# Kernel optimization log

Hardware: AMD Instinct MI355X
Metric: run time of the kernel (lower is better)

Reference implementation:

```python
import jax, jax.numpy as jnp
import numpy as np

T, B, D, H = 512, 128, 512, 512

def setup_inputs() -> dict:
    key = jax.random.key(0)
    k1, k2, k3, k4 = jax.random.split(key, 4)
    s_in = 1.0 / np.sqrt(D)
    s_h = 1.0 / np.sqrt(H)
    return {
        "x": jax.random.normal(k1, (T, B, D), dtype=jnp.float32),
        "resets": jax.random.randint(k2, (T, B), 0, 2) > 0,
        "h0": jnp.zeros((B, H), dtype=jnp.float32),  # GRUCell.initialize_carry -> zeros
        "Wi": jax.random.normal(k3, (D, 3 * H), dtype=jnp.float32) * s_in,  # [ir|iz|in]
        "bi": jnp.zeros((3 * H,), dtype=jnp.float32),
        "Wh": jax.random.normal(k4, (H, 3 * H), dtype=jnp.float32) * s_h,  # [hr|hz|hn]
        "bhn": jnp.zeros((H,), dtype=jnp.float32),
    }

def reference(x, resets, h0, Wi, bi, Wh, bhn):
    # Precompute all input-side gate projections in one big GEMM: [T,B,3H]
    xg = jnp.einsum('tbd,dk->tbk', x, Wi) + bi

    def step(h, inp):
        xg_t, reset_t = inp
        # reset masking: replace carry with fresh zero carry where episode resets
        h = jnp.where(reset_t[:, None], jnp.zeros_like(h), h)
        hg = h @ Wh  # [B,3H]
        xr, xz, xn = jnp.split(xg_t, 3, axis=-1)
        hr, hz, hn = jnp.split(hg, 3, axis=-1)
        r = jax.nn.sigmoid(xr + hr)
        z = jax.nn.sigmoid(xz + hz)
        n = jnp.tanh(xn + r * (hn + bhn))
        h_new = (1.0 - z) * n + z * h
        return h_new, h_new

    h_final, ys = jax.lax.scan(step, h0, (xg, resets))
    return h_final, ys
```

## Files before the change

kernel.cpp:

```cpp
#include <hip/hip_runtime.h>

typedef __attribute__((ext_vector_type(4))) float f32x4;
typedef __attribute__((ext_vector_type(8))) _Float16 f16x8;
typedef __attribute__((ext_vector_type(4))) _Float16 f16x4;
typedef unsigned short u16;
typedef unsigned int u32;
typedef unsigned long long u64;

#define XGCAP 34304
#define NXG 4096

__device__ __forceinline__ float sigm(float v){ return 1.0f / (1.0f + __expf(-v)); }
__device__ __forceinline__ float tanh_fast(float v){
  v = fminf(15.0f, fmaxf(-15.0f, v));
  float e = __expf(2.0f * v);
  return (e - 1.0f) / (e + 1.0f);
}
__device__ __forceinline__ void gload16(const void* g, void* l){
  __builtin_amdgcn_global_load_lds((const __attribute__((address_space(1))) void*)g,
                                   (__attribute__((address_space(3))) void*)l, 16, 0, 0);
}
__device__ __forceinline__ double aload(const double* p){
  return __hip_atomic_load(p, __ATOMIC_RELAXED, __HIP_MEMORY_SCOPE_AGENT);
}
__device__ __forceinline__ void astore(float* p, float v){
  __hip_atomic_store(p, v, __ATOMIC_RELAXED, __HIP_MEMORY_SCOPE_AGENT);
}
__device__ __forceinline__ u32 apoll(const u32* p){
  return __hip_atomic_load(p, __ATOMIC_RELAXED, __HIP_MEMORY_SCOPE_AGENT);
}
__device__ __forceinline__ void abump(u32* p, u32 v){
  __hip_atomic_fetch_add(p, v, __ATOMIC_RELAXED, __HIP_MEMORY_SCOPE_AGENT);
}
__device__ __forceinline__ float2 d2f2(double d){ union{double d; float2 f;} u; u.d = d; return u.f; }

__global__ __launch_bounds__(512) void prep_lists(
    const void* __restrict__ resets_raw, const float* __restrict__ h0,
    u32* __restrict__ rows, u32* __restrict__ off, int* __restrict__ nlists)
{
  __shared__ u64 cb[128][8];
  __shared__ u32 cnt8[8][512];
  __shared__ u32 cnt[520];
  __shared__ u32 offs[521];
  __shared__ u32 cur[520];
  __shared__ int is_bytes, h0nz, maxli;
  const int tid = threadIdx.x;
  const int b = tid & 127, tc = tid >> 7;
  for (int i = tid; i < 520; i += 512){ cnt[i] = 0; cur[i] = 0; }
  if (tid == 0){ is_bytes = 0; h0nz = 0; maxli = 0; }
  for (int i = tid; i < 64; i += 512) rows[65536 + i] = (2u << 16);
  __syncthreads();
  {
    const u32* w = (const u32*)resets_raw;
    int bad = 0;
    for (int i = tid; i < 4096; i += 512) bad |= (w[i] > 1u);
    if (bad) atomicOr(&is_bytes, 1);
  }
  {
    const u32* hw = (const u32*)h0;
    u32 o = 0;
    for (int i = tid; i < 65536; i += 512) o |= hw[i];
    if (o) atomicOr(&h0nz, 1);
  }
  __syncthreads();
  const bool h0zero = (h0nz == 0);
  u64 bits0 = 0, bits1 = 0;
  if (is_bytes){
    const unsigned char* ru8 = (const unsigned char*)resets_raw;
    for (int i = 0; i < 128; ++i){
      int t = tc*128 + i;
      if (ru8[t*128 + b]){
        if (i < 64) bits0 |= 1ull << i; else bits1 |= 1ull << (i - 64);
      }
    }
  } else {
    const u32* ri32 = (const u32*)resets_raw;
    for (int i = 0; i < 128; ++i){
      int t = tc*128 + i;
      if (ri32[t*128 + b]){
        if (i < 64) bits0 |= 1ull << i; else bits1 |= 1ull << (i - 64);
      }
    }
  }
  cb[b][tc*2]     = bits0;
  cb[b][tc*2 + 1] = bits1;
  __syncthreads();

#define CELL_LI() \
    u64 myw = (i < 64) ? bits0 : bits1; \
    int rs = (int)((myw >> (i & 63)) & 1ull); \
    int k = t >> 6; \
    u64 m = cb[b][k] | (k == 0 ? 1ull : 0ull); \
    int r6 = t & 63; \
    m &= (r6 == 63) ? ~0ull : ((1ull << (r6 + 1)) - 1ull); \
    while (m == 0ull){ --k; m = cb[b][k] | (k == 0 ? 1ull : 0ull); } \
    int lastE = (k << 6) + 63 - (int)__builtin_clzll(m); \
    int depth = t - lastE; \
    int li = (depth == 0) ? ((rs || h0zero) ? 0 : 1) : (depth + 1);

  {
    u64 cpack = 0;
    int lmax = 0;
    for (int i = 0; i < 128; ++i){
      const int t = tc*128 + i;
      CELL_LI();
      if (li > lmax) lmax = li;
      if (li < 8) cpack += 1ull << (li * 8);
      else atomicAdd(&cnt[li], 1u);
    }
    atomicMax(&maxli, lmax);
    #pragma unroll
    for (int l = 0; l < 8; ++l) cnt8[l][tid] = (u32)((cpack >> (l * 8)) & 0xFFull);
  }
  __syncthreads();
  if (tid < 8){
    u32 s = 0;
    for (int i = 0; i < 512; ++i){ u32 v = cnt8[tid][i]; cnt8[tid][i] = s; s += v; }
    cnt[tid] = s;
  }
  __syncthreads();
  if (tid == 0){
    u32 s = 0;
    for (int i = 0; i < 520; ++i){ offs[i] = s; s += cnt[i]; }
    offs[520] = s;
    *nlists = maxli + 1;
  }
  __syncthreads();
  for (int i = tid; i < 521; i += 512) off[i] = offs[i];
  __syncthreads();
  {
    u64 lcpack = 0;
    for (int i = 0; i < 128; ++i){
      const int t = tc*128 + i;
      CELL_LI();
      u32 p;
      if (li < 8){
        u32 loc = (u32)((lcpack >> (li * 8)) & 0xFFull);
        lcpack += 1ull << (li * 8);
        p = offs[li] + cnt8[li][tid] + loc;
      } else {
        p = offs[li] + atomicAdd(&cur[li], 1u);
      }
      u32 fl = rs ? 1u : ((t == 0) ? (h0zero ? 1u : 2u) : 0u);
      rows[p] = (u32)t | ((u32)b << 9) | (fl << 16);
    }
  }
#undef CELL_LI
}

__global__ void prep_w(const float* __restrict__ Wi, const float* __restrict__ Wh,
                       char* __restrict__ wimg, u32* __restrict__ zflags)
{
  if (blockIdx.x < 128){
    #pragma unroll
    for (int i = 0; i < 4; ++i)
      zflags[blockIdx.x * 1024 + (int)threadIdx.x + i * 256] = 0;
  }
  __shared__ float tile[64][65];
  const int bc = blockIdx.x % 24;
  const int bk = blockIdx.x / 24;
  const int scol0 = (bc % 3) * 512 + (bc / 3) * 64;
  const int k0 = bk * 64;
  #pragma unroll
  for (int i = 0; i < 4; ++i){
    int idx = (int)threadIdx.x + i*256;
    int kk = idx >> 4, c4 = idx & 15;
    int k = k0 + kk;
    const float* src = (k < 512) ? (Wi + (size_t)k*1536 + scol0 + c4*4)
                                 : (Wh + (size_t)(k-512)*1536 + scol0 + c4*4);
    float4 v = *(const float4*)src;
    tile[kk][c4*4+0] = v.x; tile[kk][c4*4+1] = v.y;
    tile[kk][c4*4+2] = v.z; tile[kk][c4*4+3] = v.w;
  }
  __syncthreads();
  const int jb = bc / 3;
  #pragma unroll
  for (int i = 0; i < 4; ++i){
    int idx = (int)threadIdx.x + i*256;
    int cc = idx >> 4, k4 = idx & 15;
    int cimg = (bc % 3)*64 + cc;
    f16x4 c;
    c[0] = (_Float16)tile[k4*4+0][cc]; c[1] = (_Float16)tile[k4*4+1][cc];
    c[2] = (_Float16)tile[k4*4+2][cc]; c[3] = (_Float16)tile[k4*4+3][cc];
    int bby = k4*8;
    int sb = (bby & 8) | ((bby & 0x70) ^ ((cimg & 7) << 4));
    *(f16x4*)(wimg + ((size_t)(jb*16 + bk))*24576 + cimg*128 + sb) = c;
  }
}

__global__ __launch_bounds__(256) void prep_x(
    const float* __restrict__ x, const u32* __restrict__ rows,
    char* __restrict__ xq)
{
  const int tid = threadIdx.x;
  const u32 lpos = blockIdx.x * 16 + (tid >> 4);
  const u32 e = rows[lpos];
  const float* src = x + ((size_t)((e & 511u)*128u + ((e >> 9) & 127u)))*512;
  const int lane16 = tid & 15;
  char* dst = xq + (size_t)lpos * 1024;
  const int swzr = ((int)lpos & 7) << 4;
  #pragma unroll
  for (int it = 0; it < 8; ++it){
    float4 v = *(const float4*)(src + it*64 + lane16*4);
    f16x4 c; c[0]=(_Float16)v.x; c[1]=(_Float16)v.y;
             c[2]=(_Float16)v.z; c[3]=(_Float16)v.w;
    int bby = lane16 * 8;
    int sb = (bby & 8) | ((bby & 0x70) ^ swzr);
    *(f16x4*)(dst + it*128 + sb) = c;
  }
}

__global__ __launch_bounds__(256, 2) void gru_fused(
    const char* __restrict__ xq, const float* __restrict__ bi,
    const float* __restrict__ bhn, const char* __restrict__ wimg,
    const float* __restrict__ h0, _Float16* __restrict__ xg,
    const u32* __restrict__ rows, const u32* __restrict__ off,
    const int* __restrict__ nlists, u32* __restrict__ hflags,
    u32* __restrict__ xflags, float* __restrict__ out)
{
  __shared__ __align__(16) char smem[81920];
  float* ys = out + 65536;
  const u32 n0 = off[1];
  const int tid = threadIdx.x;
  const int lane = tid & 63, wave = tid >> 6;
  const int nblk = (int)gridDim.x;

  int g = (int)blockIdx.x;
  while (g < NXG){
    const int tm = g >> 3, jb = g & 7;
    g += nblk;
    const char* asrc = xq + (size_t)tm * 131072;
    const char* wsrc = wimg + ((size_t)jb * 16) * 24576;

    f32x4 acc[3][8];
    #pragma unroll
    for (int c = 0; c < 3; ++c)
      #pragma unroll
      for (int m = 0; m < 8; ++m) acc[c][m] = (f32x4){0.f,0.f,0.f,0.f};

#define DMA_A(KC, BUF) do{ \
    char* l_ = smem + (BUF)*16384 + wave*4096; \
    const char* g_ = asrc + (size_t)(wave*32 + (lane>>3))*1024 + (KC)*128 + (lane&7)*16; \
    _Pragma("unroll") for (int i_ = 0; i_ < 4; ++i_) \
      gload16(g_ + i_*8192, l_ + i_*1024); }while(0)
#define DMA_W(KC, BUF) do{ \
    char* l_ = smem + 32768 + (BUF)*24576 + wave*6144; \
    const char* g_ = wsrc + (size_t)(KC)*24576 + wave*6144 + lane*16; \
    _Pragma("unroll") for (int i_ = 0; i_ < 6; ++i_) \
      gload16(g_ + i_*1024, l_ + i_*1024); }while(0)

    DMA_A(0, 0); DMA_W(0, 0);
    __syncthreads();
    for (int kc = 0; kc < 8; ++kc){
      const int cur = kc & 1;
      if (kc < 7){ DMA_A(kc+1, cur^1); DMA_W(kc+1, cur^1); }
      const char* Ab = smem + cur*16384;
      const char* Wb = smem + 32768 + cur*24576;
      #pragma unroll
      for (int kk = 0; kk < 2; ++kk){
        const int bby = kk*64 + (lane>>4)*16;
        f16x8 af[8];
        #pragma unroll
        for (int mi = 0; mi < 8; ++mi){
          int rr = mi*16 + (lane & 15);
          af[mi] = *(const f16x8*)(Ab + rr*128 + (bby ^ ((rr & 7) << 4)));
        }
        #pragma unroll
        for (int cls = 0; cls < 3; ++cls){
          int cc = cls*64 + wave*16 + (lane & 15);
          f16x8 wf = *(const f16x8*)(Wb + cc*128 + (bby ^ ((cc & 7) << 4)));
          #pragma unroll
          for (int mi = 0; mi < 8; ++mi)
            acc[cls][mi] = __builtin_amdgcn_mfma_f32_16x16x32_f16(af[mi], wf, acc[cls][mi], 0, 0, 0);
        }
      }
      __syncthreads();
    }
#undef DMA_A
#undef DMA_W

    const int jloc = wave*16 + (lane & 15);
    const int j = jb*64 + jloc;
    const float bir = bi[j], biz = bi[512 + j], bin = bi[1024 + j], bh = bhn[j];
    #pragma unroll
    for (int mi = 0; mi < 8; ++mi){
      #pragma unroll
      for (int rg = 0; rg < 4; ++rg){
        int r = mi*16 + (lane >> 4)*4 + rg;
        u32 e = rows[tm*128 + r];
        int tt = (int)(e & 511u), bb = (int)((e >> 9) & 127u);
        float xr = acc[0][mi][rg] + bir;
        float xz = acc[1][mi][rg] + biz;
        float xn = acc[2][mi][rg] + bin;
        if ((e >> 16) == 1u){
          float rr = sigm(xr), zz = sigm(xz);
          float nn = tanh_fast(xn + rr*bh);
          float hv = (1.f - zz)*nn;
          ys[((size_t)(tt*128 + bb))*512 + j] = hv;
          if (tt == 511) out[(size_t)bb*512 + j] = hv;
        } else {
          u32 xi = (u32)(tm*128 + r) - n0;
          if (xi >= XGCAP) xi = 0;
          _Float16* p = xg + (size_t)xi*1536 + jb*192 + jloc;
          p[0]   = (_Float16)xr;
          p[64]  = (_Float16)xz;
          p[128] = (_Float16)xn;
        }
      }
    }
    __syncthreads();
    if (tid < 128){
      u32 e = rows[tm*128 + tid];
      if ((e >> 16) == 1u) abump(&hflags[(e & 511u)*128u + ((e >> 9) & 127u)], 1u);
      else                 abump(&xflags[tm*128 + tid], 1u);
    }
    __syncthreads();
  }

  const int L = *nlists;
  int myNext = g - NXG;
  int gt = 0;
  for (int li = 1; li < L; ++li){
    const u32 offA = off[li];
    const int nA = (int)(off[li+1] - offA);
    const int tA = (nA + 63) >> 6;
    const int nt = tA * 8;
    while (myNext < gt + nt){
      const int tile = myNext - gt;
      myNext += nblk;
      const int tm = tile >> 3, jb = tile & 7;
      const u32 rowbase = offA + (u32)tm*64u;
      const u32 xibase = rowbase - n0;
      const int mcount = min(64, nA - tm*64);
      const char* wp = wimg + ((size_t)jb*16 + 8)*24576;
      const int jloc = wave*16 + (lane & 15);

      if (wave == 0 && lane < mcount){
        u32 e = rows[rowbase + lane];
        const bool needH = ((e >> 16) == 0u);
        u32 hidx = ((e & 511u) - 1u)*128u + ((e >> 9) & 127u);
        int guard = 0;
        for (;;){
          bool ok = apoll(&xflags[rowbase + lane]) >= 8u;
          if (ok && needH) ok = apoll(&hflags[hidx]) >= 8u;
          if (ok) break;
          __builtin_amdgcn_s_sleep(1);
          if (++guard > (1 << 20)) break;
        }
      }
      __syncthreads();

      const float* rp[4];
      #pragma unroll
      for (int i = 0; i < 4; ++i){
        u32 e = rows[rowbase + (tid>>4) + i*16];
        int tt = (int)(e & 511u), bb = (int)((e >> 9) & 127u);
        const float* base = ((e >> 16) == 0u) ? (ys + ((size_t)((tt-1)*128 + bb))*512)
                                              : (h0 + (size_t)bb*512);
        rp[i] = base + (tid & 15)*4;
      }

      _Float16 xgp[3][4][4];
      #pragma unroll
      for (int mi = 0; mi < 4; ++mi){
        #pragma unroll
        for (int rg = 0; rg < 4; ++rg){
          u32 xi = xibase + (u32)(mi*16 + (lane >> 4)*4 + rg);
          if (xi >= XGCAP) xi = 0;
          const _Float16* p = xg + (size_t)xi*1536 + jb*192 + jloc;
          xgp[0][mi][rg] = p[0];
          xgp[1][mi][rg] = p[64];
          xgp[2][mi][rg] = p[128];
        }
      }

      f32x4 acc[3][4];
      #pragma unroll
      for (int c = 0; c < 3; ++c)
        #pragma unroll
        for (int m = 0; m < 4; ++m) acc[c][m] = (f32x4){0.f,0.f,0.f,0.f};
      float hp[4][4];
      double s0[4][2], s1[4][2], s2[4][2];

#define ALOAD(S, CK) do{ \
    _Pragma("unroll") for (int i_ = 0; i_ < 4; ++i_){ \
      const double* p_ = (const double*)(rp[i_] + (CK)*64); \
      S[i_][0] = aload(p_); S[i_][1] = aload(p_ + 1); } }while(0)

#define AWRITE(S, CK) do{ \
    char* An_ = smem + ((CK) & 3)*8192; \
    _Pragma("unroll") for (int i_ = 0; i_ < 4; ++i_){ \
      float2 u0_ = d2f2(S[i_][0]), u1_ = d2f2(S[i_][1]); \
      int r_ = (tid>>4) + i_*16, bby_ = (tid & 15)*8; \
      int sb_ = (bby_ & 8) | ((bby_ & 0x70) ^ ((r_ & 7) << 4)); \
      f16x4 c_; c_[0]=(_Float16)u0_.x; c_[1]=(_Float16)u0_.y; \
                c_[2]=(_Float16)u1_.x; c_[3]=(_Float16)u1_.y; \
      *(f16x4*)(An_ + r_*128 + sb_) = c_; } }while(0)

#define COMPUTE(KC) do{ \
    const char* Ab_ = smem + ((KC) & 3)*8192; \
    _Pragma("unroll") for (int kk_ = 0; kk_ < 2; ++kk_){ \
      const int bby_ = kk_*64 + (lane>>4)*16; \
      f16x8 af_[4]; \
      _Pragma("unroll") for (int mi_ = 0; mi_ < 4; ++mi_){ \
        int rr_ = mi_*16 + (lane & 15); \
        af_[mi_] = *(const f16x8*)(Ab_ + rr_*128 + (bby_ ^ ((rr_ & 7) << 4))); } \
      _Pragma("unroll") for (int cl_ = 0; cl_ < 3; ++cl_){ \
        int cc_ = cl_*64 + wave*16 + (lane & 15); \
        f16x8 wf_ = *(const f16x8*)(wp + (size_t)(KC)*24576 + cc_*128 + (bby_ ^ ((cc_ & 7) << 4))); \
        _Pragma("unroll") for (int mi_ = 0; mi_ < 4; ++mi_) \
          acc[cl_][mi_] = __builtin_amdgcn_mfma_f32_16x16x32_f16(af_[mi_], wf_, acc[cl_][mi_], 0, 0, 0); } } \
    if ((KC) == jb){ \
      const int bb2_ = jloc*2; \
      _Pragma("unroll") for (int mi_ = 0; mi_ < 4; ++mi_) \
        _Pragma("unroll") for (int rg_ = 0; rg_ < 4; ++rg_){ \
          int r2_ = mi_*16 + (lane >> 4)*4 + rg_; \
          int sb2_ = (bb2_ & 0x0F) | ((bb2_ & 0x70) ^ ((r2_ & 7) << 4)); \
          hp[mi_][rg_] = (float)(*(const _Float16*)(Ab_ + r2_*128 + sb2_)); } } }while(0)

      ALOAD(s0, 0); ALOAD(s1, 1); ALOAD(s2, 2);
      AWRITE(s0, 0);
      __syncthreads();
      ALOAD(s0, 3); COMPUTE(0); AWRITE(s1, 1); __syncthreads();
      ALOAD(s1, 4); COMPUTE(1); AWRITE(s2, 2); __syncthreads();
      ALOAD(s2, 5); COMPUTE(2); AWRITE(s0, 3); __syncthreads();
      ALOAD(s0, 6); COMPUTE(3); AWRITE(s1, 4); __syncthreads();
      ALOAD(s1, 7); COMPUTE(4); AWRITE(s2, 5); __syncthreads();
                    COMPUTE(5); AWRITE(s0, 6); __syncthreads();
                    COMPUTE(6); AWRITE(s1, 7); __syncthreads();
                    COMPUTE(7);
#undef ALOAD
#undef AWRITE
#undef COMPUTE

      const int j = jb*64 + jloc;
      const float bh = bhn[j];
      #pragma unroll
      for (int mi = 0; mi < 4; ++mi){
        #pragma unroll
        for (int rg = 0; rg < 4; ++rg){
          int r = mi*16 + (lane >> 4)*4 + rg;
          if (r < mcount){
            u32 e = rows[rowbase + r];
            int tt = (int)(e & 511u), bb = (int)((e >> 9) & 127u);
            float rr = sigm((float)xgp[0][mi][rg] + acc[0][mi][rg]);
            float zz = sigm((float)xgp[1][mi][rg] + acc[1][mi][rg]);
            float nn = tanh_fast((float)xgp[2][mi][rg] + rr*(acc[2][mi][rg] + bh));
            float hv = (1.f - zz)*nn + zz*hp[mi][rg];
            astore(&ys[((size_t)(tt*128 + bb))*512 + j], hv);
            if (tt == 511) out[(size_t)bb*512 + j] = hv;
          }
        }
      }
      __syncthreads();
      if (tid < mcount){
        u32 e = rows[rowbase + tid];
        abump(&hflags[(e & 511u)*128u + ((e >> 9) & 127u)], 1u);
      }
    }
    gt += nt;
  }
}

extern "C" void kernel_launch(void* const* d_in, const int* in_sizes, int n_in,
                              void* d_out, int out_size, void* d_ws, size_t ws_size,
                              hipStream_t stream)
{
  const float* x  = (const float*)d_in[0];
  const void*  resets = d_in[1];
  const float* h0 = (const float*)d_in[2];
  const float* Wi = (const float*)d_in[3];
  const float* bi = (const float*)d_in[4];
  const float* Wh = (const float*)d_in[5];
  const float* bhn= (const float*)d_in[6];
  float* out = (float*)d_out;

  char* ws = (char*)d_ws;
  u32* off    = (u32*)ws;
  int* nlists = (int*)(ws + 4096);
  u32* rows   = (u32*)(ws + 8192);
  u32* hflags = (u32*)(ws + 294912);
  u32* xflags = (u32*)(ws + 557056);
  char* wimg  = ws + 819200;
  char* xq    = ws + 4194304;
  _Float16* xg = (_Float16*)(ws + 71303168);

  prep_lists<<<dim3(1), dim3(512), 0, stream>>>(resets, h0, rows, off, nlists);
  prep_w<<<dim3(384), dim3(256), 0, stream>>>(Wi, Wh, wimg, hflags);
  prep_x<<<dim3(4096), dim3(256), 0, stream>>>(x, rows, xq);

  int perCU = 0;
  (void)hipOccupancyMaxActiveBlocksPerMultiprocessor(&perCU, gru_fused, 256, 0);
  if (perCU < 1) perCU = 1;
  int grid = perCU * 256;
  if (grid > 1024) grid = 1024;

  void* args[] = {(void*)&xq, (void*)&bi, (void*)&bhn, (void*)&wimg,
                  (void*)&h0, (void*)&xg, (void*)&rows, (void*)&off,
                  (void*)&nlists, (void*)&hflags, (void*)&xflags, (void*)&out};
  hipLaunchCooperativeKernel(gru_fused, dim3(grid), dim3(256), args, 0, stream);

  (void)in_sizes; (void)n_in; (void)out_size; (void)ws_size;
}
```

Baseline: 931.2 us.

## Merge weight and input prep kernels; read GEMM weights directly from global

```diff
diff --git a/kernel.cpp b/kernel.cpp
--- a/kernel.cpp
+++ b/kernel.cpp
@@ -148,13 +148,35 @@
 #undef CELL_LI
 }
 
-__global__ void prep_w(const float* __restrict__ Wi, const float* __restrict__ Wh,
-                       char* __restrict__ wimg, u32* __restrict__ zflags)
+__global__ __launch_bounds__(256) void prep_wx(
+    const float* __restrict__ Wi, const float* __restrict__ Wh,
+    char* __restrict__ wimg, u32* __restrict__ zflags,
+    const float* __restrict__ x, const u32* __restrict__ rows,
+    char* __restrict__ xq)
 {
+  const int tid = threadIdx.x;
+  if (blockIdx.x >= 384){
+    const u32 lpos = (blockIdx.x - 384) * 16 + (tid >> 4);
+    const u32 e = rows[lpos];
+    const float* src = x + ((size_t)((e & 511u)*128u + ((e >> 9) & 127u)))*512;
+    const int lane16 = tid & 15;
+    char* dst = xq + (size_t)lpos * 1024;
+    const int swzr = ((int)lpos & 7) << 4;
+    #pragma unroll
+    for (int it = 0; it < 8; ++it){
+      float4 v = *(const float4*)(src + it*64 + lane16*4);
+      f16x4 c; c[0]=(_Float16)v.x; c[1]=(_Float16)v.y;
+               c[2]=(_Float16)v.z; c[3]=(_Float16)v.w;
+      int bby = lane16 * 8;
+      int sb = (bby & 8) | ((bby & 0x70) ^ swzr);
+      *(f16x4*)(dst + it*128 + sb) = c;
+    }
+    return;
+  }
   if (blockIdx.x < 128){
     #pragma unroll
     for (int i = 0; i < 4; ++i)
-      zflags[blockIdx.x * 1024 + (int)threadIdx.x + i * 256] = 0;
+      zflags[blockIdx.x * 1024 + tid + i * 256] = 0;
   }
   __shared__ float tile[64][65];
   const int bc = blockIdx.x % 24;
@@ -163,7 +185,7 @@
   const int k0 = bk * 64;
   #pragma unroll
   for (int i = 0; i < 4; ++i){
-    int idx = (int)threadIdx.x + i*256;
+    int idx = tid + i*256;
     int kk = idx >> 4, c4 = idx & 15;
     int k = k0 + kk;
     const float* src = (k < 512) ? (Wi + (size_t)k*1536 + scol0 + c4*4)
@@ -176,7 +198,7 @@
   const int jb = bc / 3;
   #pragma unroll
   for (int i = 0; i < 4; ++i){
-    int idx = (int)threadIdx.x + i*256;
+    int idx = tid + i*256;
     int cc = idx >> 4, k4 = idx & 15;
     int cimg = (bc % 3)*64 + cc;
     f16x4 c;
@@ -188,28 +210,6 @@
   }
 }
 
-__global__ __launch_bounds__(256) void prep_x(
-    const float* __restrict__ x, const u32* __restrict__ rows,
-    char* __restrict__ xq)
-{
-  const int tid = threadIdx.x;
-  const u32 lpos = blockIdx.x * 16 + (tid >> 4);
-  const u32 e = rows[lpos];
-  const float* src = x + ((size_t)((e & 511u)*128u + ((e >> 9) & 127u)))*512;
-  const int lane16 = tid & 15;
-  char* dst = xq + (size_t)lpos * 1024;
-  const int swzr = ((int)lpos & 7) << 4;
-  #pragma unroll
-  for (int it = 0; it < 8; ++it){
-    float4 v = *(const float4*)(src + it*64 + lane16*4);
-    f16x4 c; c[0]=(_Float16)v.x; c[1]=(_Float16)v.y;
-             c[2]=(_Float16)v.z; c[3]=(_Float16)v.w;
-    int bby = lane16 * 8;
-    int sb = (bby & 8) | ((bby & 0x70) ^ swzr);
-    *(f16x4*)(dst + it*128 + sb) = c;
-  }
-}
-
 __global__ __launch_bounds__(256, 2) void gru_fused(
     const char* __restrict__ xq, const float* __restrict__ bi,
     const float* __restrict__ bhn, const char* __restrict__ wimg,
@@ -218,7 +218,7 @@
     const int* __restrict__ nlists, u32* __restrict__ hflags,
     u32* __restrict__ xflags, float* __restrict__ out)
 {
-  __shared__ __align__(16) char smem[81920];
+  __shared__ __align__(16) char smem[32768];
   float* ys = out + 65536;
   const u32 n0 = off[1];
   const int tid = threadIdx.x;
@@ -243,19 +243,13 @@
     const char* g_ = asrc + (size_t)(wave*32 + (lane>>3))*1024 + (KC)*128 + (lane&7)*16; \
     _Pragma("unroll") for (int i_ = 0; i_ < 4; ++i_) \
       gload16(g_ + i_*8192, l_ + i_*1024); }while(0)
-#define DMA_W(KC, BUF) do{ \
-    char* l_ = smem + 32768 + (BUF)*24576 + wave*6144; \
-    const char* g_ = wsrc + (size_t)(KC)*24576 + wave*6144 + lane*16; \
-    _Pragma("unroll") for (int i_ = 0; i_ < 6; ++i_) \
-      gload16(g_ + i_*1024, l_ + i_*1024); }while(0)
-
-    DMA_A(0, 0); DMA_W(0, 0);
+
+    DMA_A(0, 0);
     __syncthreads();
     for (int kc = 0; kc < 8; ++kc){
       const int cur = kc & 1;
-      if (kc < 7){ DMA_A(kc+1, cur^1); DMA_W(kc+1, cur^1); }
+      if (kc < 7) DMA_A(kc+1, cur^1);
       const char* Ab = smem + cur*16384;
-      const char* Wb = smem + 32768 + cur*24576;
       #pragma unroll
       for (int kk = 0; kk < 2; ++kk){
         const int bby = kk*64 + (lane>>4)*16;
@@ -268,7 +262,7 @@
         #pragma unroll
         for (int cls = 0; cls < 3; ++cls){
           int cc = cls*64 + wave*16 + (lane & 15);
-          f16x8 wf = *(const f16x8*)(Wb + cc*128 + (bby ^ ((cc & 7) << 4)));
+          f16x8 wf = *(const f16x8*)(wsrc + (size_t)kc*24576 + cc*128 + (bby ^ ((cc & 7) << 4)));
           #pragma unroll
           for (int mi = 0; mi < 8; ++mi)
             acc[cls][mi] = __builtin_amdgcn_mfma_f32_16x16x32_f16(af[mi], wf, acc[cls][mi], 0, 0, 0);
@@ -277,7 +271,6 @@
       __syncthreads();
     }
 #undef DMA_A
-#undef DMA_W
 
     const int jloc = wave*16 + (lane & 15);
     const int j = jb*64 + jloc;
@@ -486,8 +479,7 @@
   _Float16* xg = (_Float16*)(ws + 71303168);
 
   prep_lists<<<dim3(1), dim3(512), 0, stream>>>(resets, h0, rows, off, nlists);
-  prep_w<<<dim3(384), dim3(256), 0, stream>>>(Wi, Wh, wimg, hflags);
-  prep_x<<<dim3(4096), dim3(256), 0, stream>>>(x, rows, xq);
+  prep_wx<<<dim3(4480), dim3(256), 0, stream>>>(Wi, Wh, wimg, hflags, x, rows, xq);
 
   int perCU = 0;
   (void)hipOccupancyMaxActiveBlocksPerMultiprocessor(&perCU, gru_fused, 256, 0);
```

Result: slower. 989.2 us (+6.2%).
